# Kernel optimization log

Measured on AMD Instinct MI355X. Metric: run time of the kernel, lower is better.

The kernel has to match this reference:

```python
import jax, jax.numpy as jnp
import numpy as np

NBINS = 100  # hard-coded in torch.histogram(first, 100)


def setup_inputs() -> dict:
    key = jax.random.key(0)
    k1, k2 = jax.random.split(key)
    z = jax.random.normal(k1, (100000, 16), dtype=jnp.float32)
    cluster_layer = jax.random.normal(k2, (16, 16), dtype=jnp.float32)
    return {"z": z, "cluster_layer": cluster_layer}


def _per_feature_hist(combined):
    """Equal-width per-feature histogram (torch.histogram(x, 100) semantics).
    combined: [N+C, F] -> edges [F, NBINS+1], counts [F, NBINS] (float)."""
    lo = combined.min(axis=0)          # [F]
    hi = combined.max(axis=0)          # [F]
    t = jnp.linspace(0.0, 1.0, NBINS + 1, dtype=combined.dtype)  # [NBINS+1]
    edges = lo[:, None] + (hi - lo)[:, None] * t[None, :]        # [F, NBINS+1]
    # bin assignment: left-closed bins, last bin right-closed (np/torch histogram)
    idx = jax.vmap(lambda e, v: jnp.searchsorted(e, v, side="right"),
                   in_axes=(0, 1))(edges, combined) - 1          # [F, N+C]
    idx = jnp.clip(idx, 0, NBINS - 1)
    counts = jax.vmap(lambda i: jnp.zeros((NBINS,), combined.dtype).at[i].add(1.0))(idx)
    return edges, counts


def _mass_dissimilarity(z, cluster_layer):
    N, F = z.shape
    C = cluster_layer.shape[0]
    combined = jax.lax.stop_gradient(jnp.concatenate([z, cluster_layer], axis=0))  # detach()
    edges, counts = _per_feature_hist(combined)          # [F,101], [F,100]

    # searchsorted(bins, .) - 1, per feature (side='left' like torch default)
    sample_bins = jax.vmap(lambda e, v: jnp.searchsorted(e, v, side="left"),
                           in_axes=(0, 1))(edges, z).T - 1              # [N, F]
    cluster_bins = jax.vmap(lambda e, v: jnp.searchsorted(e, v, side="left"),
                            in_axes=(0, 1))(edges, cluster_layer).T - 1  # [C, F]

    mx = jnp.maximum(sample_bins[:, None, :], cluster_bins[None, :, :])  # [N, C, F]
    mn = jnp.minimum(sample_bins[:, None, :], cluster_bins[None, :, :])  # [N, C, F]

    cum = jnp.cumsum(counts, axis=1)                     # [F, NBINS]
    f_idx = jnp.arange(F)                                # broadcasts over [N, C, F]
    is_zero = mn <= 0
    lo_idx = jnp.where(is_zero, 0, mn - 1)
    lo_sum = cum[f_idx, lo_idx]                          # [N, C, F]
    hi_sum = cum[f_idx, jnp.clip(mx, 0, NBINS - 1)]      # [N, C, F]
    sum_counts = jnp.where(is_zero, hi_sum, hi_sum - lo_sum)

    divisor = jnp.asarray(N + C, z.dtype)
    # len(counts)==1 in the original after reshape(1,1,F,NBINS), so no extra divide
    mass = jnp.sqrt(jnp.sum((sum_counts / divisor) ** 2, axis=2))  # [N, C]
    return mass


def reference(z, cluster_layer):
    # get_Q(z, 'mass'): q = 1/(1+mass), row-normalized
    q = 1.0 / (1.0 + _mass_dissimilarity(z, cluster_layer))
    q = q / jnp.sum(q, axis=1, keepdims=True)
    return q
```

## Files before the change

kernel.cpp:

```cpp
#include <hip/hip_runtime.h>
#include <stdint.h>

#define NBINS 100
#define FF 16
#define CC 16
#define MM_BLOCKS 128
#define HIST_BLOCKS 256


__device__ __forceinline__ unsigned enc_f(float v) {
    unsigned u = __float_as_uint(v);
    return (u & 0x80000000u) ? ~u : (u | 0x80000000u);
}
__device__ __forceinline__ float dec_f(unsigned e) {
    unsigned u = (e & 0x80000000u) ? (e ^ 0x80000000u) : ~u ^ 0u;
    u = (e & 0x80000000u) ? (e ^ 0x80000000u) : ~e;
    return __uint_as_float(u);
}
__device__ __forceinline__ unsigned shfl_xor_u(unsigned x, int m) {
    return (unsigned)__shfl_xor((int)x, m, 64);
}

__global__ __launch_bounds__(256) void k_minmax(const float4* __restrict__ z4,
                                                const float4* __restrict__ cl4,
                                                int zn4, int total4,
                                                unsigned* __restrict__ partials,
                                                unsigned* __restrict__ counts) {
    int gtid = blockIdx.x * 256 + threadIdx.x;
    if (gtid < FF * NBINS) counts[gtid] = 0u;

    unsigned mn[4] = {~0u, ~0u, ~0u, ~0u}, mx[4] = {0u, 0u, 0u, 0u};
    int stride = MM_BLOCKS * 256;
    for (int i = gtid; i < total4; i += stride) {
        float4 v = (i < zn4) ? z4[i] : cl4[i - zn4];
        unsigned e;
        e = enc_f(v.x); mn[0] = min(mn[0], e); mx[0] = max(mx[0], e);
        e = enc_f(v.y); mn[1] = min(mn[1], e); mx[1] = max(mx[1], e);
        e = enc_f(v.z); mn[2] = min(mn[2], e); mx[2] = max(mx[2], e);
        e = enc_f(v.w); mn[3] = min(mn[3], e); mx[3] = max(mx[3], e);
    }
#pragma unroll
    for (int off = 4; off < 64; off <<= 1) {
#pragma unroll
        for (int c = 0; c < 4; ++c) {
            mn[c] = min(mn[c], shfl_xor_u(mn[c], off));
            mx[c] = max(mx[c], shfl_xor_u(mx[c], off));
        }
    }
    __shared__ unsigned smin[4][16], smax[4][16];
    int wave = threadIdx.x >> 6, lane = threadIdx.x & 63;
    if (lane < 4) {
#pragma unroll
        for (int c = 0; c < 4; ++c) {
            smin[wave][4 * lane + c] = mn[c];
            smax[wave][4 * lane + c] = mx[c];
        }
    }
    __syncthreads();
    if (threadIdx.x < 16) {
        int f = threadIdx.x;
        partials[blockIdx.x * 32 + f] =
            min(min(smin[0][f], smin[1][f]), min(smin[2][f], smin[3][f]));
        partials[blockIdx.x * 32 + 16 + f] =
            max(max(smax[0][f], smax[1][f]), max(smax[2][f], smax[3][f]));
    }
}

__device__ __forceinline__ void build_edges(const unsigned* __restrict__ partials,
                                            unsigned* ulo, unsigned* uhi,
                                            float* se, float* ss, float* slo) {
    int t = threadIdx.x;
    if (t < 16) { ulo[t] = ~0u; uhi[t] = 0u; }
    __syncthreads();
    {
        int f = t & 15, b0 = (t >> 4) * (MM_BLOCKS / 16);
        unsigned um = ~0u, ux = 0u;
#pragma unroll
        for (int b = b0; b < b0 + MM_BLOCKS / 16; ++b) {
            um = min(um, partials[b * 32 + f]);
            ux = max(ux, partials[b * 32 + 16 + f]);
        }
        atomicMin(&ulo[f], um);
        atomicMax(&uhi[f], ux);
    }
    __syncthreads();
    for (int i = t; i < FF * (NBINS + 1); i += 256) {
        int f = i / (NBINS + 1), k = i - f * (NBINS + 1);
        float lo = dec_f(ulo[f]), hi = dec_f(uhi[f]);
        float tt = (k == NBINS) ? 1.0f : __fmul_rn((float)k, 0.01f);
        se[i] = __fadd_rn(lo, __fmul_rn(__fsub_rn(hi, lo), tt));
    }
    if (t < 16) {
        float lo = dec_f(ulo[t]), hi = dec_f(uhi[t]);
        float d = hi - lo;
        ss[t] = d > 0.0f ? 100.0f / d : 0.0f;
        slo[t] = lo;
    }
    __syncthreads();
}

__global__ __launch_bounds__(256) void k_hist(const float4* __restrict__ z4,
                                              const float4* __restrict__ cl4,
                                              int zn4, int total4,
                                              const unsigned* __restrict__ partials,
                                              unsigned* __restrict__ counts) {
    __shared__ unsigned ulo[16], uhi[16];
    __shared__ float se[FF * (NBINS + 1)];
    __shared__ float ss[16], slo[16];
    __shared__ unsigned sc[FF * NBINS];
    for (int i = threadIdx.x; i < FF * NBINS; i += 256) sc[i] = 0u;
    build_edges(partials, ulo, uhi, se, ss, slo);

    int gtid = blockIdx.x * 256 + threadIdx.x;
    int stride = HIST_BLOCKS * 256;
    int fb = (4 * gtid) & 15;
    for (int i = gtid; i < total4; i += stride) {
        float4 v4 = (i < zn4) ? z4[i] : cl4[i - zn4];
        float vv[4] = {v4.x, v4.y, v4.z, v4.w};
#pragma unroll
        for (int c = 0; c < 4; ++c) {
            int f = (fb + c) & 15;
            float v = vv[c];
            const float* ef = &se[f * (NBINS + 1)];
            int g = (int)((v - slo[f]) * ss[f]);
            g = g < 0 ? 0 : (g > NBINS - 1 ? NBINS - 1 : g);
            while (g < NBINS - 1 && ef[g + 1] <= v) ++g;
            while (g > 0 && ef[g] > v) --g;
            atomicAdd(&sc[f * NBINS + g], 1u);
        }
    }
    __syncthreads();
    for (int i = threadIdx.x; i < FF * NBINS; i += 256) {
        unsigned c = sc[i];
        if (c) atomicAdd(&counts[i], c);
    }
}

__global__ __launch_bounds__(256) void k_main(const float4* __restrict__ z4, int N,
                                              float inv_div,
                                              const unsigned* __restrict__ partials,
                                              const unsigned* __restrict__ counts,
                                              const float* __restrict__ cl,
                                              float* __restrict__ out) {
    __shared__ unsigned ulo[16], uhi[16];
    __shared__ float se[FF * (NBINS + 1)];
    __shared__ float ss[16], slo[16];
    __shared__ unsigned scnt[FF * NBINS];
    __shared__ float scum[FF * NBINS];
    __shared__ float2 sqp[CC * FF];
    int t = threadIdx.x;
    for (int i = t; i < FF * NBINS; i += 256) scnt[i] = counts[i];
    build_edges(partials, ulo, uhi, se, ss, slo);
    if (t < 16) {
        float s = 0.0f;
        const unsigned* cp = &scnt[t * NBINS];
        float* fp = &scum[t * NBINS];
#pragma unroll
        for (int k = 0; k < NBINS; ++k) { s += (float)cp[k]; fp[k] = s; }
    }
    __syncthreads();
    {
        int c = t >> 4, f = t & 15;
        float v = cl[c * FF + f];
        const float* ef = &se[f * (NBINS + 1)];
        int g = (int)((v - slo[f]) * ss[f]);
        g = g < 0 ? 0 : (g > NBINS - 1 ? NBINS - 1 : g);
        while (g < NBINS - 1 && ef[g + 1] < v) ++g;
        while (g >= 0 && ef[g] >= v) --g;
        float Qc = scum[f * NBINS + (g < 0 ? 0 : g)];
        float Pc = (g >= 1) ? scum[f * NBINS + g - 1] : 0.0f;
        sqp[t] = make_float2(Qc, Pc);
    }
    __syncthreads();

    int n = blockIdx.x * 256 + t;
    if (n >= N) return;

    float v[FF];
    const float4* zr = z4 + (size_t)n * 4;
    float4 a0 = zr[0], a1 = zr[1], a2 = zr[2], a3 = zr[3];
    v[0] = a0.x; v[1] = a0.y; v[2]  = a0.z; v[3]  = a0.w;
    v[4] = a1.x; v[5] = a1.y; v[6]  = a1.z; v[7]  = a1.w;
    v[8] = a2.x; v[9] = a2.y; v[10] = a2.z; v[11] = a2.w;
    v[12] = a3.x; v[13] = a3.y; v[14] = a3.z; v[15] = a3.w;

    float Qs[FF], Ps[FF];
#pragma unroll
    for (int f = 0; f < FF; ++f) {
        const float* ef = &se[f * (NBINS + 1)];
        int g = (int)((v[f] - slo[f]) * ss[f]);
        g = g < 0 ? 0 : (g > NBINS - 1 ? NBINS - 1 : g);
        while (g < NBINS - 1 && ef[g + 1] < v[f]) ++g;
        while (g >= 0 && ef[g] >= v[f]) --g;
        Qs[f] = scum[f * NBINS + (g < 0 ? 0 : g)];
        Ps[f] = (g >= 1) ? scum[f * NBINS + g - 1] : 0.0f;
    }

    float q[CC];
    float rowsum = 0.0f;
#pragma unroll
    for (int c = 0; c < CC; ++c) {
        float acc = 0.0f;
#pragma unroll
        for (int f = 0; f < FF; ++f) {
            float2 qp = sqp[c * FF + f];
            float h = fmaxf(Qs[f], qp.x);
            float l = fminf(Ps[f], qp.y);
            float d = h - l;
            acc = fmaf(d, d, acc);
        }
        float mass = sqrtf(acc) * inv_div;
        float qq = 1.0f / (1.0f + mass);
        q[c] = qq;
        rowsum += qq;
    }

    float* op = out + (size_t)n * CC;
    float4 o;
    o.x = q[0] / rowsum;  o.y = q[1] / rowsum;  o.z = q[2] / rowsum;  o.w = q[3] / rowsum;
    ((float4*)op)[0] = o;
    o.x = q[4] / rowsum;  o.y = q[5] / rowsum;  o.z = q[6] / rowsum;  o.w = q[7] / rowsum;
    ((float4*)op)[1] = o;
    o.x = q[8] / rowsum;  o.y = q[9] / rowsum;  o.z = q[10] / rowsum; o.w = q[11] / rowsum;
    ((float4*)op)[2] = o;
    o.x = q[12] / rowsum; o.y = q[13] / rowsum; o.z = q[14] / rowsum; o.w = q[15] / rowsum;
    ((float4*)op)[3] = o;
}

extern "C" void kernel_launch(void* const* d_in, const int* in_sizes, int n_in,
                              void* d_out, int out_size, void* d_ws, size_t ws_size,
                              hipStream_t stream) {
    const float* z  = (const float*)d_in[0];
    const float* cl = (const float*)d_in[1];
    float* out = (float*)d_out;
    int N = in_sizes[0] / FF;

    char* ws = (char*)d_ws;
    unsigned* partials = (unsigned*)(ws);
    unsigned* counts   = (unsigned*)(ws + 16384);

    int zn4 = N * FF / 4;
    int total4 = (N + CC) * FF / 4;
    float inv_div = 1.0f / (float)(N + CC);

    k_minmax<<<MM_BLOCKS, 256, 0, stream>>>((const float4*)z, (const float4*)cl,
                                            zn4, total4, partials, counts);
    k_hist<<<HIST_BLOCKS, 256, 0, stream>>>((const float4*)z, (const float4*)cl,
                                            zn4, total4, partials, counts);
    int blocks = (N + 255) / 256;
    k_main<<<blocks, 256, 0, stream>>>((const float4*)z, N, inv_div,
                                       partials, counts, cl, out);
}
```

Measured before the change: 96.82 us.

## Compute sample bins once in histogram pass and store as bytes for main kernel

The histogram kernel now also computes each element's left-side searchsorted bin and writes it as an int8 into workspace. The main kernel reads those 16 bytes per row instead of 64 bytes of z, and no longer rebuilds edges or redoes the binary search. The edge table in shared memory is replaced by computing edges on the fly. The min/max block count is doubled. The cost is an extra byte-per-element write in the histogram pass and an added dependency between kernels.

```diff
diff --git a/kernel.cpp b/kernel.cpp
--- a/kernel.cpp
+++ b/kernel.cpp
@@ -4,7 +4,7 @@
 #define NBINS 100
 #define FF 16
 #define CC 16
-#define MM_BLOCKS 128
+#define MM_BLOCKS 256
 #define HIST_BLOCKS 256
 
 
@@ -13,12 +13,15 @@
     return (u & 0x80000000u) ? ~u : (u | 0x80000000u);
 }
 __device__ __forceinline__ float dec_f(unsigned e) {
-    unsigned u = (e & 0x80000000u) ? (e ^ 0x80000000u) : ~u ^ 0u;
-    u = (e & 0x80000000u) ? (e ^ 0x80000000u) : ~e;
+    unsigned u = (e & 0x80000000u) ? (e ^ 0x80000000u) : ~e;
     return __uint_as_float(u);
 }
 __device__ __forceinline__ unsigned shfl_xor_u(unsigned x, int m) {
     return (unsigned)__shfl_xor((int)x, m, 64);
+}
+__device__ __forceinline__ float edgeval(float lo, float d, int k) {
+    float tt = (k == NBINS) ? 1.0f : __fmul_rn((float)k, 0.01f);
+    return __fadd_rn(lo, __fmul_rn(d, tt));
 }
 
 __global__ __launch_bounds__(256) void k_minmax(const float4* __restrict__ z4,
@@ -66,91 +69,84 @@
     }
 }
 
-__device__ __forceinline__ void build_edges(const unsigned* __restrict__ partials,
-                                            unsigned* ulo, unsigned* uhi,
-                                            float* se, float* ss, float* slo) {
-    int t = threadIdx.x;
-    if (t < 16) { ulo[t] = ~0u; uhi[t] = 0u; }
-    __syncthreads();
-    {
-        int f = t & 15, b0 = (t >> 4) * (MM_BLOCKS / 16);
-        unsigned um = ~0u, ux = 0u;
-#pragma unroll
-        for (int b = b0; b < b0 + MM_BLOCKS / 16; ++b) {
-            um = min(um, partials[b * 32 + f]);
-            ux = max(ux, partials[b * 32 + 16 + f]);
-        }
-        atomicMin(&ulo[f], um);
-        atomicMax(&uhi[f], ux);
-    }
-    __syncthreads();
-    for (int i = t; i < FF * (NBINS + 1); i += 256) {
-        int f = i / (NBINS + 1), k = i - f * (NBINS + 1);
-        float lo = dec_f(ulo[f]), hi = dec_f(uhi[f]);
-        float tt = (k == NBINS) ? 1.0f : __fmul_rn((float)k, 0.01f);
-        se[i] = __fadd_rn(lo, __fmul_rn(__fsub_rn(hi, lo), tt));
-    }
-    if (t < 16) {
-        float lo = dec_f(ulo[t]), hi = dec_f(uhi[t]);
-        float d = hi - lo;
-        ss[t] = d > 0.0f ? 100.0f / d : 0.0f;
-        slo[t] = lo;
-    }
-    __syncthreads();
-}
-
 __global__ __launch_bounds__(256) void k_hist(const float4* __restrict__ z4,
                                               const float4* __restrict__ cl4,
                                               int zn4, int total4,
                                               const unsigned* __restrict__ partials,
-                                              unsigned* __restrict__ counts) {
+                                              unsigned* __restrict__ counts,
+                                              unsigned* __restrict__ sb32) {
     __shared__ unsigned ulo[16], uhi[16];
-    __shared__ float se[FF * (NBINS + 1)];
-    __shared__ float ss[16], slo[16];
+    __shared__ float slo[16], sd[16], sscl[16];
     __shared__ unsigned sc[FF * NBINS];
-    for (int i = threadIdx.x; i < FF * NBINS; i += 256) sc[i] = 0u;
-    build_edges(partials, ulo, uhi, se, ss, slo);
-
-    int gtid = blockIdx.x * 256 + threadIdx.x;
+    int t = threadIdx.x;
+    for (int i = t; i < FF * NBINS; i += 256) sc[i] = 0u;
+    if (t < 16) { ulo[t] = ~0u; uhi[t] = 0u; }
+    __syncthreads();
+    {
+        int f = t & 15, b0 = (t >> 4) * (MM_BLOCKS / 16);
+        unsigned um = ~0u, ux = 0u;
+#pragma unroll
+        for (int b = b0; b < b0 + MM_BLOCKS / 16; ++b) {
+            um = min(um, partials[b * 32 + f]);
+            ux = max(ux, partials[b * 32 + 16 + f]);
+        }
+        atomicMin(&ulo[f], um);
+        atomicMax(&uhi[f], ux);
+    }
+    __syncthreads();
+    if (t < 16) {
+        float lo = dec_f(ulo[t]), hi = dec_f(uhi[t]);
+        float d = __fsub_rn(hi, lo);
+        slo[t] = lo; sd[t] = d;
+        sscl[t] = d > 0.0f ? 100.0f / d : 0.0f;
+    }
+    __syncthreads();
+
+    int gtid = blockIdx.x * 256 + t;
     int stride = HIST_BLOCKS * 256;
     int fb = (4 * gtid) & 15;
+    float lo_c[4], d_c[4], scl_c[4];
+#pragma unroll
+    for (int c = 0; c < 4; ++c) {
+        int f = (fb + c) & 15;
+        lo_c[c] = slo[f]; d_c[c] = sd[f]; scl_c[c] = sscl[f];
+    }
     for (int i = gtid; i < total4; i += stride) {
         float4 v4 = (i < zn4) ? z4[i] : cl4[i - zn4];
         float vv[4] = {v4.x, v4.y, v4.z, v4.w};
+        unsigned pack = 0u;
 #pragma unroll
         for (int c = 0; c < 4; ++c) {
             int f = (fb + c) & 15;
-            float v = vv[c];
-            const float* ef = &se[f * (NBINS + 1)];
-            int g = (int)((v - slo[f]) * ss[f]);
+            float v = vv[c], lo = lo_c[c], dd = d_c[c];
+            int g = (int)((v - lo) * scl_c[c]);
             g = g < 0 ? 0 : (g > NBINS - 1 ? NBINS - 1 : g);
-            while (g < NBINS - 1 && ef[g + 1] <= v) ++g;
-            while (g > 0 && ef[g] > v) --g;
+            while (g < NBINS - 1 && edgeval(lo, dd, g + 1) <= v) ++g;
+            while (g > 0 && edgeval(lo, dd, g) > v) --g;
             atomicAdd(&sc[f * NBINS + g], 1u);
-        }
-    }
-    __syncthreads();
-    for (int i = threadIdx.x; i < FF * NBINS; i += 256) {
+            int gl = g;
+            while (gl >= 0 && edgeval(lo, dd, gl) >= v) --gl;
+            pack |= ((unsigned)gl & 0xffu) << (8 * c);
+        }
+        sb32[i] = pack;
+    }
+    __syncthreads();
+    for (int i = t; i < FF * NBINS; i += 256) {
         unsigned c = sc[i];
         if (c) atomicAdd(&counts[i], c);
     }
 }
 
-__global__ __launch_bounds__(256) void k_main(const float4* __restrict__ z4, int N,
-                                              float inv_div,
-                                              const unsigned* __restrict__ partials,
+__global__ __launch_bounds__(256) void k_main(const signed char* __restrict__ sbins,
+                                              int N, float inv_div,
                                               const unsigned* __restrict__ counts,
-                                              const float* __restrict__ cl,
                                               float* __restrict__ out) {
-    __shared__ unsigned ulo[16], uhi[16];
-    __shared__ float se[FF * (NBINS + 1)];
-    __shared__ float ss[16], slo[16];
     __shared__ unsigned scnt[FF * NBINS];
     __shared__ float scum[FF * NBINS];
-    __shared__ float2 sqp[CC * FF];
+    __shared__ float sqpf[CC * 32];
     int t = threadIdx.x;
     for (int i = t; i < FF * NBINS; i += 256) scnt[i] = counts[i];
-    build_edges(partials, ulo, uhi, se, ss, slo);
+    __syncthreads();
     if (t < 16) {
         float s = 0.0f;
         const unsigned* cp = &scnt[t * NBINS];
@@ -161,37 +157,31 @@
     __syncthreads();
     {
         int c = t >> 4, f = t & 15;
-        float v = cl[c * FF + f];
-        const float* ef = &se[f * (NBINS + 1)];
-        int g = (int)((v - slo[f]) * ss[f]);
-        g = g < 0 ? 0 : (g > NBINS - 1 ? NBINS - 1 : g);
-        while (g < NBINS - 1 && ef[g + 1] < v) ++g;
-        while (g >= 0 && ef[g] >= v) --g;
-        float Qc = scum[f * NBINS + (g < 0 ? 0 : g)];
-        float Pc = (g >= 1) ? scum[f * NBINS + g - 1] : 0.0f;
-        sqp[t] = make_float2(Qc, Pc);
+        int g = (int)sbins[(size_t)(N + c) * FF + f];
+        sqpf[c * 32 + 2 * f]     = scum[f * NBINS + (g < 0 ? 0 : g)];
+        sqpf[c * 32 + 2 * f + 1] = (g >= 1) ? scum[f * NBINS + g - 1] : 0.0f;
     }
     __syncthreads();
 
     int n = blockIdx.x * 256 + t;
     if (n >= N) return;
 
-    float v[FF];
-    const float4* zr = z4 + (size_t)n * 4;
-    float4 a0 = zr[0], a1 = zr[1], a2 = zr[2], a3 = zr[3];
-    v[0] = a0.x; v[1] = a0.y; v[2]  = a0.z; v[3]  = a0.w;
-    v[4] = a1.x; v[5] = a1.y; v[6]  = a1.z; v[7]  = a1.w;
-    v[8] = a2.x; v[9] = a2.y; v[10] = a2.z; v[11] = a2.w;
-    v[12] = a3.x; v[13] = a3.y; v[14] = a3.z; v[15] = a3.w;
+    const int4* br = (const int4*)(sbins + (size_t)n * FF);
+    int4 w = *br;
+    int gs[FF];
+    gs[0]  = (w.x << 24) >> 24; gs[1]  = (w.x << 16) >> 24;
+    gs[2]  = (w.x << 8)  >> 24; gs[3]  =  w.x >> 24;
+    gs[4]  = (w.y << 24) >> 24; gs[5]  = (w.y << 16) >> 24;
+    gs[6]  = (w.y << 8)  >> 24; gs[7]  =  w.y >> 24;
+    gs[8]  = (w.z << 24) >> 24; gs[9]  = (w.z << 16) >> 24;
+    gs[10] = (w.z << 8)  >> 24; gs[11] =  w.z >> 24;
+    gs[12] = (w.w << 24) >> 24; gs[13] = (w.w << 16) >> 24;
+    gs[14] = (w.w << 8)  >> 24; gs[15] =  w.w >> 24;
 
     float Qs[FF], Ps[FF];
 #pragma unroll
     for (int f = 0; f < FF; ++f) {
-        const float* ef = &se[f * (NBINS + 1)];
-        int g = (int)((v[f] - slo[f]) * ss[f]);
-        g = g < 0 ? 0 : (g > NBINS - 1 ? NBINS - 1 : g);
-        while (g < NBINS - 1 && ef[g + 1] < v[f]) ++g;
-        while (g >= 0 && ef[g] >= v[f]) --g;
+        int g = gs[f];
         Qs[f] = scum[f * NBINS + (g < 0 ? 0 : g)];
         Ps[f] = (g >= 1) ? scum[f * NBINS + g - 1] : 0.0f;
     }
@@ -201,13 +191,18 @@
 #pragma unroll
     for (int c = 0; c < CC; ++c) {
         float acc = 0.0f;
-#pragma unroll
-        for (int f = 0; f < FF; ++f) {
-            float2 qp = sqp[c * FF + f];
-            float h = fmaxf(Qs[f], qp.x);
-            float l = fminf(Ps[f], qp.y);
-            float d = h - l;
-            acc = fmaf(d, d, acc);
+        const float4* qprow = (const float4*)&sqpf[c * 32];
+#pragma unroll
+        for (int f2 = 0; f2 < 8; ++f2) {
+            float4 qp = qprow[f2];
+            float h0 = fmaxf(Qs[2 * f2], qp.x);
+            float l0 = fminf(Ps[2 * f2], qp.y);
+            float d0 = h0 - l0;
+            acc = fmaf(d0, d0, acc);
+            float h1 = fmaxf(Qs[2 * f2 + 1], qp.z);
+            float l1 = fminf(Ps[2 * f2 + 1], qp.w);
+            float d1 = h1 - l1;
+            acc = fmaf(d1, d1, acc);
         }
         float mass = sqrtf(acc) * inv_div;
         float qq = 1.0f / (1.0f + mass);
@@ -236,8 +231,9 @@
     int N = in_sizes[0] / FF;
 
     char* ws = (char*)d_ws;
-    unsigned* partials = (unsigned*)(ws);
-    unsigned* counts   = (unsigned*)(ws + 16384);
+    unsigned*    partials = (unsigned*)(ws);
+    unsigned*    counts   = (unsigned*)(ws + 32768);
+    signed char* sbins    = (signed char*)(ws + 39168);
 
     int zn4 = N * FF / 4;
     int total4 = (N + CC) * FF / 4;
@@ -246,8 +242,8 @@
     k_minmax<<<MM_BLOCKS, 256, 0, stream>>>((const float4*)z, (const float4*)cl,
                                             zn4, total4, partials, counts);
     k_hist<<<HIST_BLOCKS, 256, 0, stream>>>((const float4*)z, (const float4*)cl,
-                                            zn4, total4, partials, counts);
+                                            zn4, total4, partials, counts,
+                                            (unsigned*)sbins);
     int blocks = (N + 255) / 256;
-    k_main<<<blocks, 256, 0, stream>>>((const float4*)z, N, inv_div,
-                                       partials, counts, cl, out);
-}
+    k_main<<<blocks, 256, 0, stream>>>(sbins, N, inv_div, counts, out);
+}
```

Measured after the change: 106.4 us. 9.9% more time.
